# Kernel optimization log

Hardware: AMD Instinct MI355X
Metric: run time of the kernel (lower is better)

The kernel has to match this reference:

```python
import jax, jax.numpy as jnp
from jax import lax
import numpy as np

# NOTE: the original module calls an opaque CUDA 'approximate dot-product' conv kernel.
# Its backward uses EXACT conv2d gradients for input/weight, so the reference forward
# math is the exact conv2d the kernel approximates. `approximate` is a learned scalar
# controlling the hardware approximation level; it does not change the exact-math output.

STRIDE = 1
PAD = (1, 1)  # (padH, padW)


def setup_inputs() -> dict:
    key = jax.random.key(0)
    k1, k2, k3 = jax.random.split(key, 3)
    B, Cin, H, W = 32, 128, 56, 56
    Cout, K = 256, 3
    x = jax.random.normal(k1, (B, Cin, H, W), dtype=jnp.float32)
    # weight init: uniform(-1, 1) per reset_parameters
    weight = jax.random.uniform(k2, (Cout, Cin, K, K), dtype=jnp.float32, minval=-1.0, maxval=1.0)
    fan_in = Cin * K * K
    bound = 1.0 / np.sqrt(fan_in)
    bias = jax.random.uniform(k3, (Cout,), dtype=jnp.float32, minval=-bound, maxval=bound)
    approximate = jnp.ones((1,), dtype=jnp.float32)
    return {"x": x, "weight": weight, "bias": bias, "approximate": approximate}


def reference(x, weight, bias, approximate):
    # Exact conv2d, NCHW input, OIHW kernel. `approximate` controls only the
    # hardware approximation level in the original CUDA kernel.
    out = lax.conv_general_dilated(
        x, weight,
        window_strides=(STRIDE, STRIDE),
        padding=((PAD[0], PAD[0]), (PAD[1], PAD[1])),
        dimension_numbers=("NCHW", "OIHW", "NCHW"),
    )
    return out + bias.reshape(1, -1, 1, 1)
```

## Files before the change

### kernel.cpp

```cpp
#include <hip/hip_runtime.h>


typedef __attribute__((ext_vector_type(8))) short short8;
typedef __attribute__((ext_vector_type(4))) float floatx4;

typedef __attribute__((address_space(1))) const void* gas_ptr;
typedef __attribute__((address_space(3))) void* las_ptr;

__device__ static inline void gl2lds16(const void* g, void* l) {
    __builtin_amdgcn_global_load_lds((gas_ptr)g, (las_ptr)l, 16, 0, 0);
}

__device__ static inline float bf2f(unsigned short u) {
    union { unsigned int i; float f; } x; x.i = ((unsigned int)u) << 16; return x.f;
}
__device__ static inline unsigned short f2bf(float f) {
    union { float f; unsigned int i; } x; x.f = f;
    unsigned int r = (x.i + 0x7FFFu + ((x.i >> 16) & 1u)) >> 16;
    return (unsigned short)r;
}

__global__ void detect_dtype(const unsigned int* __restrict__ x,
                             unsigned int* __restrict__ flag) {
    int cnt = 0;
    for (int r = 0; r < 4; ++r) {
        unsigned int w = x[r * 64 + threadIdx.x];
        unsigned short lo = (unsigned short)(w & 0xFFFFu);
        int e = (lo >> 7) & 0xFF;
        bool plaus = (lo == 0) || (e >= 96 && e <= 144);
        unsigned long long b = __ballot(plaus);
        if (threadIdx.x == 0) cnt += (int)__popcll(b);
    }
    if (threadIdx.x == 0) *flag = (cnt >= 205) ? 1u : 0u;
}

__global__ void wt_repack(const void* __restrict__ wsrc,
                          unsigned short* __restrict__ wt,
                          const unsigned int* __restrict__ flag) {
    const bool isbf = (*flag != 0);
    int idx = blockIdx.x * 256 + threadIdx.x;
    int ci  = idx & 127;
    int co  = (idx >> 7) & 255;
    int off = idx >> 15;
    size_t s = (size_t)(co * 128 + ci) * 9 + off;
    float v = isbf ? bf2f(((const unsigned short*)wsrc)[s])
                   : ((const float*)wsrc)[s];
    wt[idx] = f2bf(v);
}

__global__ void x_repack(const void* __restrict__ xsrc,
                         unsigned short* __restrict__ xp,
                         const unsigned int* __restrict__ flag) {
    const bool isbf = (*flag != 0);
    int bh  = blockIdx.x;
    int b   = bh / 58, hp = bh - b * 58;
    int tid = threadIdx.x;
    unsigned short* row = xp + (size_t)(b * 58 + hp) * 58 * 128;
    uint4 z; z.x = z.y = z.z = z.w = 0u;
    if (hp == 0 || hp == 57) {
        uint4* r = (uint4*)row;
        for (int t = tid; t < 928; t += 256) r[t] = z;
        return;
    }
    int h = hp - 1;
    if (tid < 16)      ((uint4*)row)[tid] = z;
    else if (tid < 32) ((uint4*)(row + 57 * 128))[tid - 16] = z;
    const size_t base = (size_t)b * 128 * 3136 + (size_t)h * 56;
    for (int t = tid; t < 896; t += 256) {
        int c = t / 56, w = t - c * 56;
        union { unsigned short s[8]; uint4 v; } pk;
#pragma unroll
        for (int j = 0; j < 8; ++j) {
            size_t idx = base + (size_t)(c * 8 + j) * 3136 + w;
            float v = isbf ? bf2f(((const unsigned short*)xsrc)[idx])
                           : ((const float*)xsrc)[idx];
            pk.s[j] = f2bf(v);
        }
        *(uint4*)(row + (w + 1) * 128 + c * 8) = pk.v;
    }
}

__global__ __launch_bounds__(256) void conv_mfma(
    const unsigned short* __restrict__ xp,
    const unsigned short* __restrict__ wt,
    const void* __restrict__ bias,
    void* __restrict__ out,
    const unsigned int* __restrict__ flag)
{
    __shared__ __align__(16) char lds[16384];
    const bool isbf = (*flag != 0);
    const int tid   = threadIdx.x;
    const int lane  = tid & 63;
    const int wv    = tid >> 6;
    const int ntile = blockIdx.x;
    const int mtile = blockIdx.y;

    const int p  = lane & 3;
    const int r0 = wv * 16 + (lane >> 2);
    const int r1 = r0 + 64;
    const int c0 = p ^ ((r0 >> 1) & 3);
    const int c1 = p ^ ((r1 >> 1) & 3);

    const unsigned short* a0 = wt + (mtile * 128 + r0) * 128 + c0 * 8;
    const unsigned short* a1 = wt + (mtile * 128 + r1) * 128 + c1 * 8;

    const int n0 = ntile * 128 + r0;
    const int n1 = ntile * 128 + r1;
    const int b0 = n0 / 3136, s0 = n0 - b0 * 3136;
    const int h0 = s0 / 56,   w0 = s0 - h0 * 56;
    const int b1 = n1 / 3136, s1 = n1 - b1 * 3136;
    const int h1 = s1 / 56,   w1 = s1 - h1 * 56;
    const unsigned short* bp0 = xp + ((size_t)(b0 * 58 + h0) * 58 + w0) * 128 + c0 * 8;
    const unsigned short* bp1 = xp + ((size_t)(b1 * 58 + h1) * 58 + w1) * 128 + c1 * 8;

    char* ldsA0 = lds + wv * 1024;
    char* ldsA1 = lds + (wv + 4) * 1024;
    char* ldsB0 = lds + 8192 + wv * 1024;
    char* ldsB1 = lds + 8192 + (wv + 4) * 1024;

    const int mbase = (wv >> 1) * 64 + (lane & 15);
    const int nbase = (wv & 1) * 64 + (lane & 15);
    const int ph    = (lane >> 4) ^ (((lane & 15) >> 1) & 3);
    const char* la = lds;
    const char* lb = lds + 8192;

    floatx4 acc[4][4] = {};

    for (int step = 0; step < 36; ++step) {
        const int off = step >> 2;
        const int kb  = (step & 3) << 5;
        const int dh  = off / 3, dw = off - dh * 3;
        const int aoff = off * 32768 + kb;
        const int boff = (dh * 58 + dw) * 128 + kb;
        gl2lds16(a0 + aoff, ldsA0);
        gl2lds16(a1 + aoff, ldsA1);
        gl2lds16(bp0 + boff, ldsB0);
        gl2lds16(bp1 + boff, ldsB1);
        __syncthreads();

        short8 af[4], bf[4];
#pragma unroll
        for (int t = 0; t < 4; ++t) {
            af[t] = *(const short8*)(la + (mbase + t * 16) * 64 + ph * 16);
            bf[t] = *(const short8*)(lb + (nbase + t * 16) * 64 + ph * 16);
        }
#pragma unroll
        for (int i = 0; i < 4; ++i)
#pragma unroll
            for (int j = 0; j < 4; ++j)
                acc[i][j] = __builtin_amdgcn_mfma_f32_16x16x32_bf16(
                    af[i], bf[j], acc[i][j], 0, 0, 0);
        __syncthreads();
    }

    const int q = lane >> 4;
#pragma unroll
    for (int j = 0; j < 4; ++j) {
        const int n = ntile * 128 + (wv & 1) * 64 + j * 16 + (lane & 15);
        const int b = n / 3136;
        const int s = n - b * 3136;
#pragma unroll
        for (int i = 0; i < 4; ++i) {
            const int co = mtile * 128 + (wv >> 1) * 64 + i * 16 + q * 4;
            float bv[4];
            if (isbf) {
                const ushort4 bb = *(const ushort4*)((const unsigned short*)bias + co);
                bv[0] = bf2f(bb.x); bv[1] = bf2f(bb.y);
                bv[2] = bf2f(bb.z); bv[3] = bf2f(bb.w);
            } else {
                const float4 bb = *(const float4*)((const float*)bias + co);
                bv[0] = bb.x; bv[1] = bb.y; bv[2] = bb.z; bv[3] = bb.w;
            }
#pragma unroll
            for (int r = 0; r < 4; ++r) {
                const float v = acc[i][j][r] + bv[r];
                const size_t o = (size_t)b * 802816 + (size_t)(co + r) * 3136 + s;
                if (isbf) ((unsigned short*)out)[o] = f2bf(v);
                else      ((float*)out)[o] = v;
            }
        }
    }
}

__global__ void conv_naive(const float* __restrict__ x,
                           const float* __restrict__ w,
                           const float* __restrict__ bias,
                           float* __restrict__ out) {
    long long i = (long long)blockIdx.x * 256 + threadIdx.x;
    if (i >= 25690112LL) return;
    int wo = (int)(i % 56); long long t = i / 56;
    int ho = (int)(t % 56); t /= 56;
    int co = (int)(t % 256); int b = (int)(t / 256);
    float acc = bias[co];
    for (int ci = 0; ci < 128; ++ci)
        for (int dh = 0; dh < 3; ++dh) {
            int hi = ho + dh - 1; if ((unsigned)hi >= 56u) continue;
            for (int dw = 0; dw < 3; ++dw) {
                int wi = wo + dw - 1; if ((unsigned)wi >= 56u) continue;
                acc += x[((size_t)(b * 128 + ci) * 56 + hi) * 56 + wi] *
                       w[((co * 128 + ci) * 3 + dh) * 3 + dw];
            }
        }
    out[i] = acc;
}

extern "C" void kernel_launch(void* const* d_in, const int* in_sizes, int n_in,
                              void* d_out, int out_size, void* d_ws, size_t ws_size,
                              hipStream_t stream) {
    const void* x    = d_in[0];
    const void* w    = d_in[1];
    const void* bias = d_in[2];

    const size_t xp_bytes = (size_t)32 * 58 * 58 * 128 * 2;
    const size_t wt_off   = xp_bytes;
    const size_t wt_bytes = (size_t)9 * 256 * 128 * 2;
    const size_t fl_off   = wt_off + wt_bytes;
    const size_t need     = fl_off + 64;

    if (ws_size >= need) {
        unsigned short* xp = (unsigned short*)d_ws;
        unsigned short* wt = (unsigned short*)((char*)d_ws + wt_off);
        unsigned int* flag = (unsigned int*)((char*)d_ws + fl_off);
        detect_dtype<<<1, 64, 0, stream>>>((const unsigned int*)x, flag);
        x_repack<<<32 * 58, 256, 0, stream>>>(x, xp, flag);
        wt_repack<<<1152, 256, 0, stream>>>(w, wt, flag);
        dim3 grid(784, 2, 1);
        conv_mfma<<<grid, 256, 0, stream>>>(xp, wt, bias, d_out, flag);
    } else {
        conv_naive<<<(25690112 + 255) / 256, 256, 0, stream>>>(
            (const float*)x, (const float*)w, (const float*)bias, (float*)d_out);
    }
}
```

Before: 253.5 us.

## Double K-tile depth in conv MFMA loop and transpose input via LDS in repack

The conv main loop now loads 64-wide K slices per step instead of 32, halving the number of barrier-separated steps (18 instead of 36) and doubling LDS to 32KB with a new XOR swizzle over 8 chunks. The input repack kernel now reads contiguous vectorized rows along width and transposes through a shared-memory tile, instead of doing strided scalar gathers across channels. Together these aim to cut sync overhead in the GEMM loop and make the NCHW-to-NHWC repack coalesced, at the cost of more LDS per block and possibly lower occupancy.

```diff
diff --git a/kernel.cpp b/kernel.cpp
--- a/kernel.cpp
+++ b/kernel.cpp
@@ -48,35 +48,64 @@
     wt[idx] = f2bf(v);
 }
 
-__global__ void x_repack(const void* __restrict__ xsrc,
-                         unsigned short* __restrict__ xp,
-                         const unsigned int* __restrict__ flag) {
+__global__ __launch_bounds__(256) void x_repack(
+    const void* __restrict__ xsrc, unsigned short* __restrict__ xp,
+    const unsigned int* __restrict__ flag) {
+    __shared__ unsigned short tile[56 * 130];
     const bool isbf = (*flag != 0);
-    int bh  = blockIdx.x;
-    int b   = bh / 58, hp = bh - b * 58;
-    int tid = threadIdx.x;
+    const int bh  = blockIdx.x;
+    const int b   = bh / 58, hp = bh - b * 58;
+    const int tid = threadIdx.x;
     unsigned short* row = xp + (size_t)(b * 58 + hp) * 58 * 128;
-    uint4 z; z.x = z.y = z.z = z.w = 0u;
     if (hp == 0 || hp == 57) {
+        uint4 z; z.x = z.y = z.z = z.w = 0u;
         uint4* r = (uint4*)row;
         for (int t = tid; t < 928; t += 256) r[t] = z;
         return;
     }
-    int h = hp - 1;
-    if (tid < 16)      ((uint4*)row)[tid] = z;
-    else if (tid < 32) ((uint4*)(row + 57 * 128))[tid - 16] = z;
-    const size_t base = (size_t)b * 128 * 3136 + (size_t)h * 56;
-    for (int t = tid; t < 896; t += 256) {
-        int c = t / 56, w = t - c * 56;
-        union { unsigned short s[8]; uint4 v; } pk;
-#pragma unroll
-        for (int j = 0; j < 8; ++j) {
-            size_t idx = base + (size_t)(c * 8 + j) * 3136 + w;
-            float v = isbf ? bf2f(((const unsigned short*)xsrc)[idx])
-                           : ((const float*)xsrc)[idx];
-            pk.s[j] = f2bf(v);
-        }
-        *(uint4*)(row + (w + 1) * 128 + c * 8) = pk.v;
+    const int h = hp - 1;
+    if (isbf) {
+        const unsigned short* xs =
+            (const unsigned short*)xsrc + (size_t)b * 128 * 3136 + h * 56;
+#pragma unroll
+        for (int it = 0; it < 7; ++it) {
+            int idx = it * 256 + tid;
+            int ci = idx / 14, w4 = idx - ci * 14;
+            ushort4 v = *(const ushort4*)(xs + (size_t)ci * 3136 + w4 * 4);
+            tile[(w4 * 4 + 0) * 130 + ci] = v.x;
+            tile[(w4 * 4 + 1) * 130 + ci] = v.y;
+            tile[(w4 * 4 + 2) * 130 + ci] = v.z;
+            tile[(w4 * 4 + 3) * 130 + ci] = v.w;
+        }
+    } else {
+        const float* xs = (const float*)xsrc + (size_t)b * 128 * 3136 + h * 56;
+#pragma unroll
+        for (int it = 0; it < 7; ++it) {
+            int idx = it * 256 + tid;
+            int ci = idx / 14, w4 = idx - ci * 14;
+            float4 v = *(const float4*)(xs + (size_t)ci * 3136 + w4 * 4);
+            tile[(w4 * 4 + 0) * 130 + ci] = f2bf(v.x);
+            tile[(w4 * 4 + 1) * 130 + ci] = f2bf(v.y);
+            tile[(w4 * 4 + 2) * 130 + ci] = f2bf(v.z);
+            tile[(w4 * 4 + 3) * 130 + ci] = f2bf(v.w);
+        }
+    }
+    __syncthreads();
+#pragma unroll
+    for (int it = 0; it < 4; ++it) {
+        int k = it * 256 + tid;
+        if (k >= 928) break;
+        int wq = k >> 4, cc = k & 15;
+        uint4 v;
+        if (wq == 0 || wq == 57) { v.x = v.y = v.z = v.w = 0u; }
+        else {
+            const unsigned short* p = &tile[(wq - 1) * 130 + cc * 8];
+            union { unsigned short s[8]; uint4 u; } pk;
+#pragma unroll
+            for (int j = 0; j < 8; ++j) pk.s[j] = p[j];
+            v = pk.u;
+        }
+        *(uint4*)(row + wq * 128 + cc * 8) = v;
     }
 }
 
@@ -87,7 +116,7 @@
     void* __restrict__ out,
     const unsigned int* __restrict__ flag)
 {
-    __shared__ __align__(16) char lds[16384];
+    __shared__ __align__(16) char lds[32768];
     const bool isbf = (*flag != 0);
     const int tid   = threadIdx.x;
     const int lane  = tid & 63;
@@ -95,65 +124,62 @@
     const int ntile = blockIdx.x;
     const int mtile = blockIdx.y;
 
-    const int p  = lane & 3;
-    const int r0 = wv * 16 + (lane >> 2);
-    const int r1 = r0 + 64;
-    const int c0 = p ^ ((r0 >> 1) & 3);
-    const int c1 = p ^ ((r1 >> 1) & 3);
-
-    const unsigned short* a0 = wt + (mtile * 128 + r0) * 128 + c0 * 8;
-    const unsigned short* a1 = wt + (mtile * 128 + r1) * 128 + c1 * 8;
-
-    const int n0 = ntile * 128 + r0;
-    const int n1 = ntile * 128 + r1;
-    const int b0 = n0 / 3136, s0 = n0 - b0 * 3136;
-    const int h0 = s0 / 56,   w0 = s0 - h0 * 56;
-    const int b1 = n1 / 3136, s1 = n1 - b1 * 3136;
-    const int h1 = s1 / 56,   w1 = s1 - h1 * 56;
-    const unsigned short* bp0 = xp + ((size_t)(b0 * 58 + h0) * 58 + w0) * 128 + c0 * 8;
-    const unsigned short* bp1 = xp + ((size_t)(b1 * 58 + h1) * 58 + w1) * 128 + c1 * 8;
-
-    char* ldsA0 = lds + wv * 1024;
-    char* ldsA1 = lds + (wv + 4) * 1024;
-    char* ldsB0 = lds + 8192 + wv * 1024;
-    char* ldsB1 = lds + 8192 + (wv + 4) * 1024;
+    const int srow  = wv * 8 + (lane >> 3);
+    const int cphys = lane & 7;
+    const int clog  = cphys ^ (srow & 7);
+
+    const unsigned short* aBase = wt + (mtile * 128 + srow) * 128 + clog * 8;
+
+    size_t bOff[4];
+#pragma unroll
+    for (int i = 0; i < 4; ++i) {
+        const int n = ntile * 128 + i * 32 + srow;
+        const int b = n / 3136, s = n - b * 3136;
+        const int h = s / 56,   w = s - h * 56;
+        bOff[i] = ((size_t)(b * 58 + h) * 58 + w) * 128 + clog * 8;
+    }
 
     const int mbase = (wv >> 1) * 64 + (lane & 15);
     const int nbase = (wv & 1) * 64 + (lane & 15);
-    const int ph    = (lane >> 4) ^ (((lane & 15) >> 1) & 3);
+    const int q     = lane >> 4;
+    const int rx    = lane & 7;
     const char* la = lds;
-    const char* lb = lds + 8192;
+    const char* lb = lds + 16384;
 
     floatx4 acc[4][4] = {};
 
-    for (int step = 0; step < 36; ++step) {
-        const int off = step >> 2;
-        const int kb  = (step & 3) << 5;
+    for (int step = 0; step < 18; ++step) {
+        const int off = step >> 1;
+        const int kb  = (step & 1) << 6;
         const int dh  = off / 3, dw = off - dh * 3;
         const int aoff = off * 32768 + kb;
-        const int boff = (dh * 58 + dw) * 128 + kb;
-        gl2lds16(a0 + aoff, ldsA0);
-        gl2lds16(a1 + aoff, ldsA1);
-        gl2lds16(bp0 + boff, ldsB0);
-        gl2lds16(bp1 + boff, ldsB1);
+        const size_t boff = (size_t)(dh * 58 + dw) * 128 + kb;
+#pragma unroll
+        for (int i = 0; i < 4; ++i) {
+            gl2lds16(aBase + i * 4096 + aoff, lds + i * 4096 + wv * 1024);
+            gl2lds16(xp + bOff[i] + boff, lds + 16384 + i * 4096 + wv * 1024);
+        }
         __syncthreads();
 
-        short8 af[4], bf[4];
-#pragma unroll
-        for (int t = 0; t < 4; ++t) {
-            af[t] = *(const short8*)(la + (mbase + t * 16) * 64 + ph * 16);
-            bf[t] = *(const short8*)(lb + (nbase + t * 16) * 64 + ph * 16);
-        }
-#pragma unroll
-        for (int i = 0; i < 4; ++i)
-#pragma unroll
-            for (int j = 0; j < 4; ++j)
-                acc[i][j] = __builtin_amdgcn_mfma_f32_16x16x32_bf16(
-                    af[i], bf[j], acc[i][j], 0, 0, 0);
+#pragma unroll
+        for (int s = 0; s < 2; ++s) {
+            const int pc = ((s * 4 + q) ^ rx) * 16;
+            short8 af[4], bfr[4];
+#pragma unroll
+            for (int t = 0; t < 4; ++t) {
+                af[t]  = *(const short8*)(la + (mbase + t * 16) * 128 + pc);
+                bfr[t] = *(const short8*)(lb + (nbase + t * 16) * 128 + pc);
+            }
+#pragma unroll
+            for (int i = 0; i < 4; ++i)
+#pragma unroll
+                for (int j = 0; j < 4; ++j)
+                    acc[i][j] = __builtin_amdgcn_mfma_f32_16x16x32_bf16(
+                        af[i], bfr[j], acc[i][j], 0, 0, 0);
+        }
         __syncthreads();
     }
 
-    const int q = lane >> 4;
 #pragma unroll
     for (int j = 0; j < 4; ++j) {
         const int n = ntile * 128 + (wv & 1) * 64 + j * 16 + (lane & 15);
```

Result: faster. 232.5 us (-8.3%).
